# Optimization experiments

Hardware: AMD Instinct MI355X
Metric: run time of the kernel (lower is better)

The kernel has to match this reference:

```python
import jax, jax.numpy as jnp
import numpy as np

B, L = 2, 2048
D_MODEL, D_INNER, D_STATE, DT_RANK, D_CONV, DEPTH = 1024, 2048, 16, 64, 4, 2
EPS = 1e-5


def setup_inputs() -> dict:
    key = jax.random.key(0)
    ks = jax.random.split(key, 8)
    rn = lambda k, s, scale=0.02: jax.random.normal(k, s, jnp.float32) * scale
    return {
        "x": jax.random.normal(ks[0], (B, L, D_MODEL), jnp.float32),
        "x_size": L,  # truthiness flag only; unused in the math
        "norm_w": jnp.ones((DEPTH, D_MODEL), jnp.float32),
        "norm_b": jnp.zeros((DEPTH, D_MODEL), jnp.float32),
        "in_proj_w": rn(ks[1], (DEPTH, 2 * D_INNER, D_MODEL)),
        "conv_w": rn(ks[2], (DEPTH, D_INNER, 1, D_CONV), 0.1),
        "conv_b": jnp.zeros((DEPTH, D_INNER), jnp.float32),
        "x_proj_w": rn(ks[3], (DEPTH, DT_RANK + 2 * D_STATE, D_INNER)),
        "dt_proj_w": rn(ks[4], (DEPTH, D_INNER, DT_RANK), 0.1),
        "dt_proj_b": jnp.full((DEPTH, D_INNER), -4.0, jnp.float32),  # softplus -> small dt
        "A_log": jnp.broadcast_to(
            jnp.log(jnp.arange(1, D_STATE + 1, dtype=jnp.float32)), (DEPTH, D_INNER, D_STATE)
        ) + jnp.zeros((DEPTH, D_INNER, D_STATE), jnp.float32),
        "D": jnp.ones((DEPTH, D_INNER), jnp.float32),
        "out_proj_w": rn(ks[5], (DEPTH, D_MODEL, D_INNER)),
    }


def _layernorm(x, w, b):
    mu = x.mean(-1, keepdims=True)
    var = ((x - mu) ** 2).mean(-1, keepdims=True)
    return (x - mu) * jax.lax.rsqrt(var + EPS) * w + b


def _selective_scan(u, dt, A, Bm, Cm, Dp):
    # u, dt: (B, L, di); A: (di, n); Bm, Cm: (B, L, n); Dp: (di,)
    def step(h, inp):
        u_t, dt_t, B_t, C_t = inp  # (B,di), (B,di), (B,n), (B,n)
        dA = jnp.exp(dt_t[..., None] * A)                       # (B, di, n)
        h = dA * h + (dt_t * u_t)[..., None] * B_t[:, None, :]  # (B, di, n)
        y = jnp.einsum('bdn,bn->bd', h, C_t)
        return h, y

    h0 = jnp.zeros((u.shape[0], A.shape[0], A.shape[1]), u.dtype)
    xs = (u.swapaxes(0, 1), dt.swapaxes(0, 1), Bm.swapaxes(0, 1), Cm.swapaxes(0, 1))
    _, ys = jax.lax.scan(step, h0, xs)  # ys: (L, B, di)
    return ys.swapaxes(0, 1) + u * Dp


def _mamba(x, in_proj_w, conv_w, conv_b, x_proj_w, dt_proj_w, dt_proj_b, A_log, Dp, out_proj_w):
    xz = jnp.einsum('bld,ed->ble', x, in_proj_w)  # (B, L, 2*di)
    u, z = jnp.split(xz, 2, axis=-1)
    # causal depthwise conv1d, kernel D_CONV
    uc = jax.lax.conv_general_dilated(
        u.swapaxes(1, 2), conv_w, (1,), [(D_CONV - 1, 0)],
        feature_group_count=D_INNER, dimension_numbers=('NCH', 'OIH', 'NCH'))
    u = jax.nn.silu(uc.swapaxes(1, 2) + conv_b)
    x_dbl = jnp.einsum('bld,ed->ble', u, x_proj_w)
    dt_r, Bm, Cm = jnp.split(x_dbl, [DT_RANK, DT_RANK + D_STATE], axis=-1)
    dt = jax.nn.softplus(jnp.einsum('blr,dr->bld', dt_r, dt_proj_w) + dt_proj_b)
    A = -jnp.exp(A_log)
    y = _selective_scan(u, dt, A, Bm, Cm, Dp)
    y = y * jax.nn.silu(z)
    return jnp.einsum('bld,ed->ble', y, out_proj_w)


def reference(x, x_size, norm_w, norm_b, in_proj_w, conv_w, conv_b, x_proj_w,
              dt_proj_w, dt_proj_b, A_log, D, out_proj_w):
    # BasicLayer passes x_size as `residual` (non-None), so each Block reduces to
    # x <- Mamba(LN(x)); the returned residual is discarded by x = blk(...)[0].
    h = x
    for i in range(DEPTH):
        hn = _layernorm(h, norm_w[i], norm_b[i])
        h = _mamba(hn, in_proj_w[i], conv_w[i], conv_b[i], x_proj_w[i],
                   dt_proj_w[i], dt_proj_b[i], A_log[i], D[i], out_proj_w[i])
    return h
```

## Files before the change

kernel.cpp:

```cpp
#include <hip/hip_runtime.h>
#include <hip/hip_bf16.h>
#include <math.h>

#define BQ 2
#define LQ 2048
#define D_MODEL 1024
#define D_INNER 2048
#define D_STATE 16
#define DT_RANK 64
#define D_CONV 4
#define DEPTH 2
#define NCHUNK 64
#define CHUNK 32
#define XSPLITK 8
#define XKC (D_INNER / XSPLITK)
#define OSK 2

typedef __attribute__((ext_vector_type(8))) short short8v;
typedef __attribute__((ext_vector_type(4))) float f32x4;

__device__ __forceinline__ short f2bf(float f) {
    union { float f; unsigned u; } v; v.f = f;
    unsigned r = v.u + 0x7fffu + ((v.u >> 16) & 1u);
    return (short)(r >> 16);
}

__device__ __forceinline__ float bf2f(unsigned short s) {
    union { unsigned u; float f; } v; v.u = ((unsigned)s) << 16;
    return v.f;
}

__device__ __forceinline__ void async16(void* lds, const void* gp) {
    __builtin_amdgcn_global_load_lds(
        (const __attribute__((address_space(1))) void*)gp,
        (__attribute__((address_space(3))) void*)lds, 16, 0, 0);
}

__global__ __launch_bounds__(256) void layernorm_kernel(
    const float* __restrict__ x, const float* __restrict__ w,
    const float* __restrict__ b, short* __restrict__ out)
{
    __shared__ float red[8];
    int row = blockIdx.x;
    const float* xr = x + (size_t)row * D_MODEL;
    float v[4];
    float s = 0.f, sq = 0.f;
#pragma unroll
    for (int i = 0; i < 4; ++i) {
        v[i] = xr[threadIdx.x + i * 256];
        s += v[i];
        sq += v[i] * v[i];
    }
#pragma unroll
    for (int off = 32; off; off >>= 1) {
        s += __shfl_down(s, off, 64);
        sq += __shfl_down(sq, off, 64);
    }
    int wid = threadIdx.x >> 6, lane = threadIdx.x & 63;
    if (!lane) { red[wid] = s; red[4 + wid] = sq; }
    __syncthreads();
    s = red[0] + red[1] + red[2] + red[3];
    sq = red[4] + red[5] + red[6] + red[7];
    float mu = s * (1.f / D_MODEL);
    float var = sq * (1.f / D_MODEL) - mu * mu;
    float rstd = rsqrtf(var + 1e-5f);
#pragma unroll
    for (int i = 0; i < 4; ++i) {
        int c = threadIdx.x + i * 256;
        out[(size_t)row * D_MODEL + c] = f2bf((v[i] - mu) * rstd * w[c] + b[c]);
    }
}

__global__ __launch_bounds__(512) void gemm256_bf16_kernel(
    const short* __restrict__ A, const short* __restrict__ W,
    short* __restrict__ C, int M, int N, int K)
{
    __shared__ __align__(16) short lds[65536];
    const int tid = threadIdx.x;
    const int lane = tid & 63;
    const int w = tid >> 6;
    const int wr = w >> 2, wc = w & 3;

    int nbx = N >> 8;
    int nwg = (M >> 8) * nbx;
    int q = nwg >> 3;
    int wg = ((int)blockIdx.x & 7) * q + ((int)blockIdx.x >> 3);
    int bx = wg % nbx, by = wg / nbx;
    int bm = by << 8, bn = bx << 8;

    const int fr = lane & 15;
    const int kl = lane >> 4;
    const int srow = lane >> 3;
    const int schunk = (lane & 7) ^ (srow & 7);

    f32x4 acc[8][4] = {};
    short8v af[4][2], bfA[2][2], bfB[2][2];

    auto STAGE = [&](int isA, int buf, int half, int kt) {
        const short* gp = isA ? A : W;
        int tile0 = isA ? bm : bn;
        int base = (isA ? 0 : 32768) + (buf * 2 + half) * 8192;
        int ko = kt << 6;
#pragma unroll
        for (int s = 0; s < 2; ++s) {
            int row = half * 128 + s * 64 + w * 8 + srow;
            const short* src = gp + (size_t)(tile0 + row) * K + ko + schunk * 8;
            async16(&lds[base + s * 4096 + w * 512], src);
        }
    };

    auto LOAD_A = [&](int buf, int mh) {
        int abase = (buf * 2 + mh) * 8192;
#pragma unroll
        for (int i = 0; i < 4; ++i) {
            int rl = wr * 64 + i * 16 + fr;
            int rsw = rl & 7;
#pragma unroll
            for (int ks = 0; ks < 2; ++ks)
                af[i][ks] = *(const short8v*)&lds[abase + rl * 64 + (((ks * 4 + kl) ^ rsw) * 8)];
        }
    };
    auto LOAD_B = [&](int buf, int nh, short8v (&bf)[2][2]) {
        int bbase = 32768 + (buf * 2 + nh) * 8192;
#pragma unroll
        for (int j = 0; j < 2; ++j) {
            int rl = wc * 32 + j * 16 + fr;
            int rsw = rl & 7;
#pragma unroll
            for (int ks = 0; ks < 2; ++ks)
                bf[j][ks] = *(const short8v*)&lds[bbase + rl * 64 + (((ks * 4 + kl) ^ rsw) * 8)];
        }
    };
    auto MFMA_Q = [&](int mh, int nh, short8v (&bf)[2][2]) {
        __builtin_amdgcn_s_setprio(1);
#pragma unroll
        for (int i = 0; i < 4; ++i)
#pragma unroll
            for (int j = 0; j < 2; ++j)
#pragma unroll
                for (int ks = 0; ks < 2; ++ks)
                    acc[mh * 4 + i][nh * 2 + j] = __builtin_amdgcn_mfma_f32_16x16x32_bf16(
                        af[i][ks], bf[j][ks], acc[mh * 4 + i][nh * 2 + j], 0, 0, 0);
        __builtin_amdgcn_s_setprio(0);
    };

#define GBAR  __builtin_amdgcn_s_barrier(); __builtin_amdgcn_sched_barrier(0);
#define LGKM  asm volatile("s_waitcnt lgkmcnt(0)" ::: "memory"); __builtin_amdgcn_sched_barrier(0);

    STAGE(1, 0, 0, 0); STAGE(0, 0, 0, 0);
    STAGE(1, 0, 1, 0); STAGE(0, 0, 1, 0);
    STAGE(1, 1, 0, 1); STAGE(0, 1, 0, 1);

    int T = K >> 7;
    for (int t = 0; t < T; ++t) {
        int last = (t == T - 1);
        asm volatile("s_waitcnt vmcnt(4)" ::: "memory");
        STAGE(1, 1, 1, 2 * t + 1);
        GBAR;
        LOAD_A(0, 0); LOAD_B(0, 0, bfA);
        LGKM; MFMA_Q(0, 0, bfA);
        GBAR;
        STAGE(0, 1, 1, 2 * t + 1);
        GBAR;
        LOAD_B(0, 1, bfB);
        LGKM; MFMA_Q(0, 1, bfB);
        GBAR;
        if (!last) STAGE(1, 0, 0, 2 * t + 2);
        GBAR;
        LOAD_A(0, 1);
        LGKM; MFMA_Q(1, 1, bfB);
        GBAR;
        if (!last) STAGE(0, 0, 0, 2 * t + 2);
        GBAR;
        MFMA_Q(1, 0, bfA);
        GBAR;
        if (last) { asm volatile("s_waitcnt vmcnt(0)" ::: "memory"); }
        else      { asm volatile("s_waitcnt vmcnt(4)" ::: "memory"); }
        if (!last) STAGE(1, 0, 1, 2 * t + 2);
        GBAR;
        LOAD_A(1, 0); LOAD_B(1, 0, bfA);
        LGKM; MFMA_Q(0, 0, bfA);
        GBAR;
        if (!last) STAGE(0, 0, 1, 2 * t + 2);
        GBAR;
        LOAD_B(1, 1, bfB);
        LGKM; MFMA_Q(0, 1, bfB);
        GBAR;
        if (!last) STAGE(1, 1, 0, 2 * t + 3);
        GBAR;
        LOAD_A(1, 1);
        LGKM; MFMA_Q(1, 1, bfB);
        GBAR;
        if (!last) STAGE(0, 1, 0, 2 * t + 3);
        GBAR;
        MFMA_Q(1, 0, bfA);
        GBAR;
    }
#undef GBAR
#undef LGKM

    int cr = (lane >> 4) * 4, cc = lane & 15;
#pragma unroll
    for (int i8 = 0; i8 < 8; ++i8) {
        int mh = i8 >> 2, ii = i8 & 3;
        int row0 = bm + mh * 128 + wr * 64 + ii * 16 + cr;
#pragma unroll
        for (int p = 0; p < 4; ++p) {
            short* Cp = C + (size_t)(row0 + p) * N + bn;
#pragma unroll
            for (int j4 = 0; j4 < 4; ++j4) {
                int nh = j4 >> 1, jj = j4 & 1;
                Cp[nh * 128 + wc * 32 + jj * 16 + cc] = f2bf(acc[i8][j4][p]);
            }
        }
    }
}

__global__ __launch_bounds__(256) void gemm_bf16_kernel(
    const short* __restrict__ A, const short* __restrict__ W,
    void* __restrict__ Cv, int M, int N, int K,
    const float* __restrict__ bias, int epilogue, int nsk)
{
    __shared__ __align__(16) short As[2][128 * 64];
    __shared__ __align__(16) short Bs[2][128 * 64];
    int tid = threadIdx.x;
    int lane = tid & 63, wv = tid >> 6;
    int nbx = N >> 7;
    int nwg = (M >> 7) * nbx;
    int ntot = nwg * nsk;
    int q = ntot >> 3;
    int wgz = ((int)blockIdx.x & 7) * q + ((int)blockIdx.x >> 3);
    int sk = wgz / nwg;
    int wg = wgz % nwg;
    int bx = wg % nbx, by = wg / nbx;
    int bm = by * 128, bn = bx * 128;
    int wr = wv >> 1, wc = wv & 1;
    int Kl = K / nsk;
    int koff = sk * Kl;

    const int fr = lane & 15;
    const int kl = lane >> 4;
    const int srow = lane >> 3;
    const int schunk = (lane & 7) ^ (srow & 7);

    f32x4 acc[4][4] = {};

    const short* Ab = A + (size_t)bm * K + koff;
    const short* Bb = W + (size_t)bn * K + koff;

    auto STAGE = [&](int buf, int kt) {
        int ko = kt << 6;
#pragma unroll
        for (int s = 0; s < 4; ++s) {
            int row = s * 32 + wv * 8 + srow;
            async16(&As[buf][s * 2048 + wv * 512], Ab + (size_t)row * K + ko + schunk * 8);
            async16(&Bs[buf][s * 2048 + wv * 512], Bb + (size_t)row * K + ko + schunk * 8);
        }
    };

    int NT = Kl >> 6;
    STAGE(0, 0);
    if (NT > 1) STAGE(1, 1);

    for (int t = 0; t < NT; ++t) {
        if (t + 1 < NT) { asm volatile("s_waitcnt vmcnt(8)" ::: "memory"); }
        else            { asm volatile("s_waitcnt vmcnt(0)" ::: "memory"); }
        __builtin_amdgcn_s_barrier();
        __builtin_amdgcn_sched_barrier(0);
        int buf = t & 1;
        short8v af[4][2], bf[4][2];
#pragma unroll
        for (int i = 0; i < 4; ++i) {
            int rl = wr * 64 + i * 16 + fr;
            int rsw = rl & 7;
#pragma unroll
            for (int ks = 0; ks < 2; ++ks)
                af[i][ks] = *(const short8v*)&As[buf][rl * 64 + (((ks * 4 + kl) ^ rsw) * 8)];
        }
#pragma unroll
        for (int j = 0; j < 4; ++j) {
            int rl = wc * 64 + j * 16 + fr;
            int rsw = rl & 7;
#pragma unroll
            for (int ks = 0; ks < 2; ++ks)
                bf[j][ks] = *(const short8v*)&Bs[buf][rl * 64 + (((ks * 4 + kl) ^ rsw) * 8)];
        }
        asm volatile("s_waitcnt lgkmcnt(0)" ::: "memory");
        __builtin_amdgcn_sched_barrier(0);
        __builtin_amdgcn_s_setprio(1);
#pragma unroll
        for (int i = 0; i < 4; ++i)
#pragma unroll
            for (int j = 0; j < 4; ++j)
#pragma unroll
                for (int ks = 0; ks < 2; ++ks)
                    acc[i][j] = __builtin_amdgcn_mfma_f32_16x16x32_bf16(
                        af[i][ks], bf[j][ks], acc[i][j], 0, 0, 0);
        __builtin_amdgcn_s_setprio(0);
        __builtin_amdgcn_s_barrier();
        __builtin_amdgcn_sched_barrier(0);
        if (t + 2 < NT) STAGE(buf, t + 2);
    }

    int cr = (lane >> 4) * 4, cc = lane & 15;
    size_t skoff = (size_t)sk * M * N;
#pragma unroll
    for (int i = 0; i < 4; ++i)
#pragma unroll
        for (int p = 0; p < 4; ++p) {
            int row = bm + wr * 64 + i * 16 + cr + p;
#pragma unroll
            for (int j = 0; j < 4; ++j) {
                int col = bn + wc * 64 + cc + j * 16;
                float v = acc[i][j][p];
                if (epilogue == 2)
                    ((short*)Cv)[(size_t)row * N + col] = f2bf(v);
                else
                    ((float*)Cv)[skoff + (size_t)row * N + col] = v;
            }
        }
}

__global__ __launch_bounds__(256) void osum_kernel(
    const float* __restrict__ P, float* __restrict__ out)
{
    size_t i = ((size_t)blockIdx.x * 256 + threadIdx.x) * 4;
    float4 a = *(const float4*)(P + i);
    float4 b = *(const float4*)(P + (size_t)BQ * LQ * D_MODEL + i);
    a.x += b.x; a.y += b.y; a.z += b.z; a.w += b.w;
    *(float4*)(out + i) = a;
}

__global__ __launch_bounds__(256) void dtproj_kernel(
    const short* __restrict__ A, const short* __restrict__ W,
    const float* __restrict__ bias, short* __restrict__ Out)
{
    int lane = threadIdx.x & 63, w = threadIdx.x >> 6;
    int m0 = blockIdx.y * 64 + w * 16;
    int bn = blockIdx.x * 128;
    int fr = lane & 15, fk = (lane >> 4) * 8;
    const short* Ap = A + (size_t)(m0 + fr) * DT_RANK + fk;
    short8v a0 = *(const short8v*)(Ap);
    short8v a1 = *(const short8v*)(Ap + 32);
    f32x4 acc[8] = {};
#pragma unroll
    for (int j = 0; j < 8; ++j) {
        const short* Wp = W + (size_t)(bn + j * 16 + fr) * DT_RANK + fk;
        short8v b0 = *(const short8v*)(Wp);
        short8v b1 = *(const short8v*)(Wp + 32);
        acc[j] = __builtin_amdgcn_mfma_f32_16x16x32_bf16(a0, b0, acc[j], 0, 0, 0);
        acc[j] = __builtin_amdgcn_mfma_f32_16x16x32_bf16(a1, b1, acc[j], 0, 0, 0);
    }
    int cr = (lane >> 4) * 4, cc = lane & 15;
#pragma unroll
    for (int j = 0; j < 8; ++j) {
        int col = bn + j * 16 + cc;
        float bv = bias[col];
#pragma unroll
        for (int p = 0; p < 4; ++p) {
            float v = acc[j][p] + bv;
            v = (v > 20.f) ? v : __logf(1.f + __expf(v));
            Out[(size_t)(m0 + cr + p) * D_INNER + col] = f2bf(v);
        }
    }
}

__global__ __launch_bounds__(256) void xproj_kernel(
    const short* __restrict__ A, const short* __restrict__ W,
    float* __restrict__ Xpart)
{
    int lane = threadIdx.x & 63, wv = threadIdx.x >> 6;
    int sk = blockIdx.x;
    int m0 = blockIdx.y * 64 + wv * 16;
    int fr = lane & 15, fk = (lane >> 4) * 8;
    const short* Ap = A + (size_t)(m0 + fr) * D_INNER + sk * XKC + fk;
    const short* Wp = W + (size_t)fr * D_INNER + sk * XKC + fk;
    f32x4 acc[6] = {};
    for (int k = 0; k < XKC; k += 32) {
        short8v af = *(const short8v*)(Ap + k);
#pragma unroll
        for (int j = 0; j < 6; ++j) {
            short8v bf = *(const short8v*)(Wp + (size_t)j * 16 * D_INNER + k);
            acc[j] = __builtin_amdgcn_mfma_f32_16x16x32_bf16(af, bf, acc[j], 0, 0, 0);
        }
    }
    int cr = (lane >> 4) * 4, cc = lane & 15;
    float* Op = Xpart + ((size_t)sk * (BQ * LQ) + m0 + cr) * 96 + cc;
#pragma unroll
    for (int j = 0; j < 6; ++j)
#pragma unroll
        for (int p = 0; p < 4; ++p)
            Op[(size_t)p * 96 + j * 16] = acc[j][p];
}

__global__ __launch_bounds__(256) void xreduce_kernel(
    const float* __restrict__ Xpart, float* __restrict__ xdbl,
    short* __restrict__ dtr)
{
    size_t i = (size_t)blockIdx.x * 256 + threadIdx.x;
    float s = 0.f;
#pragma unroll
    for (int sk = 0; sk < XSPLITK; ++sk)
        s += Xpart[(size_t)sk * ((size_t)BQ * LQ * 96) + i];
    xdbl[i] = s;
    int col = (int)(i % 96);
    if (col < DT_RANK)
        dtr[(i / 96) * DT_RANK + col] = f2bf(s);
}

__global__ __launch_bounds__(256) void conv_silu_kernel(
    const unsigned short* __restrict__ uz, short* __restrict__ outb,
    const float* __restrict__ w, const float* __restrict__ bias)
{
    int idx = blockIdx.x * 256 + threadIdx.x;
    int c = idx & (D_INNER - 1);
    int bl = idx / D_INNER;
    int l = bl & (LQ - 1);
    int b = bl / LQ;
    float acc = bias[c];
#pragma unroll
    for (int k = 0; k < D_CONV; ++k) {
        int ls = l - (D_CONV - 1) + k;
        if (ls >= 0)
            acc += bf2f(uz[((size_t)b * LQ + ls) * (2 * D_INNER) + c]) * w[c * D_CONV + k];
    }
    float val = acc / (1.f + __expf(-acc));
    outb[idx] = f2bf(val);
}

__global__ __launch_bounds__(256) void scan_phase1_kernel(
    const unsigned short* __restrict__ u, const unsigned short* __restrict__ dt,
    const float* __restrict__ xdbl, const float* __restrict__ A_log,
    float* __restrict__ Pbuf, float* __restrict__ Fbuf)
{
    __shared__ float S[CHUNK][D_STATE];
    int t = threadIdx.x;
    int d = blockIdx.x * 256 + t;
    int c = blockIdx.y;
    int b = blockIdx.z;
    int l0 = c * CHUNK;
    {
        int row = t >> 3, cc2 = (t & 7) * 2;
        const float* src = xdbl + ((size_t)(b * LQ + l0 + row)) * 96 + DT_RANK + cc2;
        *(float2*)&S[row][cc2] = *(const float2*)src;
    }
    float A[D_STATE], h[D_STATE];
    {
        const float4* ap = (const float4*)(A_log + (size_t)d * D_STATE);
#pragma unroll
        for (int g = 0; g < 4; ++g) {
            float4 a = ap[g];
            A[g*4+0] = -__expf(a.x); A[g*4+1] = -__expf(a.y);
            A[g*4+2] = -__expf(a.z); A[g*4+3] = -__expf(a.w);
        }
    }
#pragma unroll
    for (int n = 0; n < D_STATE; ++n) h[n] = 0.f;
    float dtsum = 0.f;
    const unsigned short* up  = u  + ((size_t)b * LQ + l0) * D_INNER + d;
    const unsigned short* dtp = dt + ((size_t)b * LQ + l0) * D_INNER + d;
    __syncthreads();

    for (int lb = 0; lb < CHUNK; lb += 8) {
        float uvv[8], dtvv[8];
#pragma unroll
        for (int i = 0; i < 8; ++i) {
            uvv[i]  = bf2f(up [(size_t)(lb + i) * D_INNER]);
            dtvv[i] = bf2f(dtp[(size_t)(lb + i) * D_INNER]);
        }
#pragma unroll
        for (int i = 0; i < 8; ++i) {
            int l = lb + i;
            float dtv = dtvv[i];
            float du = dtv * uvv[i];
            dtsum += dtv;
#pragma unroll
            for (int n4 = 0; n4 < D_STATE; n4 += 4) {
                float4 Bv = *(const float4*)&S[l][n4];
                float bb[4] = {Bv.x, Bv.y, Bv.z, Bv.w};
#pragma unroll
                for (int k = 0; k < 4; ++k) {
                    int n = n4 + k;
                    float dA = __expf(dtv * A[n]);
                    h[n] = dA * h[n] + du * bb[k];
                }
            }
        }
    }
    size_t base = ((size_t)(b * NCHUNK + c) * D_STATE) * D_INNER + d;
#pragma unroll
    for (int n = 0; n < D_STATE; ++n) {
        Pbuf[base + (size_t)n * D_INNER] = __expf(A[n] * dtsum);
        Fbuf[base + (size_t)n * D_INNER] = h[n];
    }
}

__global__ __launch_bounds__(256) void scan_phase2_kernel(
    const float* __restrict__ Pbuf, float* __restrict__ Fbuf)
{
    int d = blockIdx.x * 256 + threadIdx.x;
    int n = blockIdx.y;
    int b = blockIdx.z;
    float hinit = 0.f;
    for (int c = 0; c < NCHUNK; ++c) {
        size_t idx = ((size_t)(b * NCHUNK + c) * D_STATE + n) * D_INNER + d;
        float P = Pbuf[idx];
        float F = Fbuf[idx];
        Fbuf[idx] = hinit;
        hinit = P * hinit + F;
    }
}

__global__ __launch_bounds__(256) void scan_phase3_kernel(
    const unsigned short* __restrict__ u, const unsigned short* __restrict__ dt,
    const float* __restrict__ xdbl, const float* __restrict__ A_log,
    const float* __restrict__ Dp, const float* __restrict__ Hinit,
    const unsigned short* __restrict__ uz, short* __restrict__ yout)
{
    __shared__ float S[CHUNK][32];
    int t = threadIdx.x;
    int d = blockIdx.x * 256 + t;
    int c = blockIdx.y;
    int b = blockIdx.z;
    int l0 = c * CHUNK;
    {
        int row = t >> 3, cg = (t & 7) * 4;
        const float* src = xdbl + ((size_t)(b * LQ + l0 + row)) * 96 + DT_RANK + cg;
        *(float4*)&S[row][cg ^ ((row & 7) << 2)] = *(const float4*)src;
    }
    float A[D_STATE], h[D_STATE];
    {
        const float4* ap = (const float4*)(A_log + (size_t)d * D_STATE);
#pragma unroll
        for (int g = 0; g < 4; ++g) {
            float4 a = ap[g];
            A[g*4+0] = -__expf(a.x); A[g*4+1] = -__expf(a.y);
            A[g*4+2] = -__expf(a.z); A[g*4+3] = -__expf(a.w);
        }
    }
    size_t base = ((size_t)(b * NCHUNK + c) * D_STATE) * D_INNER + d;
#pragma unroll
    for (int n = 0; n < D_STATE; ++n)
        h[n] = Hinit[base + (size_t)n * D_INNER];
    float Dd = Dp[d];
    const unsigned short* up  = u  + ((size_t)b * LQ + l0) * D_INNER + d;
    const unsigned short* dtp = dt + ((size_t)b * LQ + l0) * D_INNER + d;
    const unsigned short* zp = uz + ((size_t)b * LQ + l0) * (2 * D_INNER) + D_INNER + d;
    short* yp = yout + ((size_t)b * LQ + l0) * D_INNER + d;
    __syncthreads();

    for (int lb = 0; lb < CHUNK; lb += 8) {
        float uvv[8], dtvv[8], zvv[8];
#pragma unroll
        for (int i = 0; i < 8; ++i) {
            uvv[i]  = bf2f(up [(size_t)(lb + i) * D_INNER]);
            dtvv[i] = bf2f(dtp[(size_t)(lb + i) * D_INNER]);
            zvv[i]  = bf2f(zp [(size_t)(lb + i) * (2 * D_INNER)]);
        }
#pragma unroll
        for (int i = 0; i < 8; ++i) {
            int l = lb + i;
            float dtv = dtvv[i];
            float du = dtv * uvv[i];
            float acc = 0.f;
            int sw = (l & 7) << 2;
#pragma unroll
            for (int n4 = 0; n4 < D_STATE; n4 += 4) {
                float4 Bv = *(const float4*)&S[l][n4 ^ sw];
                float4 Cv = *(const float4*)&S[l][(16 + n4) ^ sw];
                float bb[4] = {Bv.x, Bv.y, Bv.z, Bv.w};
                float cc[4] = {Cv.x, Cv.y, Cv.z, Cv.w};
#pragma unroll
                for (int k = 0; k < 4; ++k) {
                    int n = n4 + k;
                    float dA = __expf(dtv * A[n]);
                    h[n] = dA * h[n] + du * bb[k];
                    acc += h[n] * cc[k];
                }
            }
            float y = acc + uvv[i] * Dd;
            float zv = zvv[i];
            float g = zv / (1.f + __expf(-zv));
            yp[(size_t)l * D_INNER] = f2bf(y * g);
        }
    }
}

__global__ __launch_bounds__(256) void convert_all_kernel(
    const float* __restrict__ w_in, const float* __restrict__ w_out,
    const float* __restrict__ w_xp, const float* __restrict__ w_dt,
    short* __restrict__ wbuf)
{
    const int IN_B  = (2 * D_INNER * D_MODEL) / 1024;
    const int OUT_B = (D_MODEL * D_INNER) / 1024;
    const int XP_B  = (96 * D_INNER) / 1024;
    int blk = blockIdx.x;
    const float* src; short* dst;
    if (blk < IN_B)                 { src = w_in;  dst = wbuf; }
    else if (blk < IN_B + OUT_B)    { src = w_out; dst = wbuf + 2 * D_INNER * D_MODEL; blk -= IN_B; }
    else if (blk < IN_B + OUT_B + XP_B) { src = w_xp; dst = wbuf + 2 * D_INNER * D_MODEL + D_MODEL * D_INNER; blk -= IN_B + OUT_B; }
    else { src = w_dt; dst = wbuf + 2 * D_INNER * D_MODEL + D_MODEL * D_INNER + 96 * D_INNER; blk -= IN_B + OUT_B + XP_B; }
    int i = blk * 1024 + threadIdx.x * 4;
    float4 v = *(const float4*)(src + i);
    short4 o = make_short4(f2bf(v.x), f2bf(v.y), f2bf(v.z), f2bf(v.w));
    *(short4*)(dst + i) = o;
}

extern "C" void kernel_launch(void* const* d_in, const int* in_sizes, int n_in,
                              void* d_out, int out_size, void* d_ws, size_t ws_size,
                              hipStream_t stream)
{
    const float* x        = (const float*)d_in[0];
    const float* norm_w   = (const float*)d_in[2];
    const float* norm_b   = (const float*)d_in[3];
    const float* in_proj  = (const float*)d_in[4];
    const float* conv_w   = (const float*)d_in[5];
    const float* conv_b   = (const float*)d_in[6];
    const float* x_proj   = (const float*)d_in[7];
    const float* dt_proj  = (const float*)d_in[8];
    const float* dt_projb = (const float*)d_in[9];
    const float* A_log    = (const float*)d_in[10];
    const float* Dp       = (const float*)d_in[11];
    const float* out_proj = (const float*)d_in[12];
    float* out = (float*)d_out;
    float* ws  = (float*)d_ws;

    const size_t BL   = (size_t)BQ * LQ;
    const size_t BLDM = BL * D_MODEL;
    const size_t BLDI = BL * D_INNER;
    const int IN_W  = 2 * D_INNER * D_MODEL;
    const int OUT_W = D_MODEL * D_INNER;
    const int XP_W  = 96 * D_INNER;
    const int DT_W  = D_INNER * DT_RANK;
    const int CV_BLOCKS = (IN_W + OUT_W + XP_W + DT_W) / 1024;

    size_t o = 0;
    float* Pbuf  = ws + o; o += BLDM;
    short* uzb   = (short*)(ws + o); o += BL * 2 * D_INNER / 2;
    short* dtb   = (short*)(ws + o); o += BLDI / 2;
    float* xdbl  = ws + o; o += BL * 96;
    float* h1    = ws + o; o += BLDM;
    float* Fbuf  = ws + o; o += BLDM;
    short* ucx   = (short*)(ws + o); o += BLDI / 2;
    short* dtr   = (short*)(ws + o); o += BL * DT_RANK / 2;
    float* Opart = ws + o; o += (size_t)OSK * BLDM;
    short* wbuf  = (short*)(ws + o);
    o += (size_t)(IN_W + OUT_W + XP_W + DT_W + 1) / 2;

    short* hnb = (short*)Pbuf;
    float* Xpart = h1;

    for (int layer = 0; layer < DEPTH; ++layer) {
        const float* src = (layer == 0) ? x : h1;
        float* dst = (layer == DEPTH - 1) ? out : h1;

        layernorm_kernel<<<(int)BL, 256, 0, stream>>>(
            src, norm_w + (size_t)layer * D_MODEL, norm_b + (size_t)layer * D_MODEL, hnb);

        convert_all_kernel<<<CV_BLOCKS, 256, 0, stream>>>(
            in_proj + (size_t)layer * IN_W, out_proj + (size_t)layer * OUT_W,
            x_proj + (size_t)layer * XP_W, dt_proj + (size_t)layer * DT_W, wbuf);

        gemm256_bf16_kernel<<<(int)(BL / 256) * (2 * D_INNER / 256), 512, 0, stream>>>(
            hnb, wbuf, uzb, (int)BL, 2 * D_INNER, D_MODEL);

        conv_silu_kernel<<<(int)(BLDI / 256), 256, 0, stream>>>(
            (const unsigned short*)uzb, ucx,
            conv_w + (size_t)layer * D_INNER * D_CONV,
            conv_b + (size_t)layer * D_INNER);

        xproj_kernel<<<dim3(XSPLITK, BL / 64), 256, 0, stream>>>(
            ucx, wbuf + IN_W + OUT_W, Xpart);
        xreduce_kernel<<<(int)(BL * 96 / 256), 256, 0, stream>>>(Xpart, xdbl, dtr);

        dtproj_kernel<<<dim3(D_INNER / 128, BL / 64), 256, 0, stream>>>(
            dtr, wbuf + IN_W + OUT_W + XP_W,
            dt_projb + (size_t)layer * D_INNER, dtb);

        const float* Al = A_log + (size_t)layer * D_INNER * D_STATE;
        scan_phase1_kernel<<<dim3(D_INNER / 256, NCHUNK, BQ), 256, 0, stream>>>(
            (const unsigned short*)ucx, (const unsigned short*)dtb, xdbl, Al, Pbuf, Fbuf);
        scan_phase2_kernel<<<dim3(D_INNER / 256, D_STATE, BQ), 256, 0, stream>>>(
            Pbuf, Fbuf);
        scan_phase3_kernel<<<dim3(D_INNER / 256, NCHUNK, BQ), 256, 0, stream>>>(
            (const unsigned short*)ucx, (const unsigned short*)dtb, xdbl, Al,
            Dp + (size_t)layer * D_INNER, Fbuf,
            (const unsigned short*)uzb, (short*)ucx);

        gemm_bf16_kernel<<<(int)(BL / 128) * (D_MODEL / 128) * OSK, 256, 0, stream>>>(
            ucx, wbuf + IN_W, Opart, (int)BL, D_MODEL, D_INNER, nullptr, 0, OSK);
        osum_kernel<<<(int)(BLDM / 1024), 256, 0, stream>>>(Opart, dst);
    }
}
```

Before: 484.0 us.

## Fuse split-K output sum with next-layer layernorm; drop Pbuf, vectorize conv

For the inter-layer boundary, the split-K partial sum of the out-projection is fused with the next layer's layernorm, so the fp32 hidden state is never written and reread. The scan no longer stores a per-state decay buffer. Phase 1 writes one dtsum per channel and chunk, and phase 2 recomputes exp(A*dtsum), which trades memory traffic for extra exp work. The conv+SiLU kernel now handles two channels per thread with 32-bit loads and stores, and the workspace layout is reorganized to match.

```diff
diff --git a/kernel.cpp b/kernel.cpp
--- a/kernel.cpp
+++ b/kernel.cpp
@@ -48,6 +48,43 @@
 #pragma unroll
     for (int i = 0; i < 4; ++i) {
         v[i] = xr[threadIdx.x + i * 256];
+        s += v[i];
+        sq += v[i] * v[i];
+    }
+#pragma unroll
+    for (int off = 32; off; off >>= 1) {
+        s += __shfl_down(s, off, 64);
+        sq += __shfl_down(sq, off, 64);
+    }
+    int wid = threadIdx.x >> 6, lane = threadIdx.x & 63;
+    if (!lane) { red[wid] = s; red[4 + wid] = sq; }
+    __syncthreads();
+    s = red[0] + red[1] + red[2] + red[3];
+    sq = red[4] + red[5] + red[6] + red[7];
+    float mu = s * (1.f / D_MODEL);
+    float var = sq * (1.f / D_MODEL) - mu * mu;
+    float rstd = rsqrtf(var + 1e-5f);
+#pragma unroll
+    for (int i = 0; i < 4; ++i) {
+        int c = threadIdx.x + i * 256;
+        out[(size_t)row * D_MODEL + c] = f2bf((v[i] - mu) * rstd * w[c] + b[c]);
+    }
+}
+
+__global__ __launch_bounds__(256) void osum_ln_kernel(
+    const float* __restrict__ P, const float* __restrict__ w,
+    const float* __restrict__ b, short* __restrict__ out)
+{
+    __shared__ float red[8];
+    int row = blockIdx.x;
+    const float* p0 = P + (size_t)row * D_MODEL;
+    const float* p1 = P + (size_t)BQ * LQ * D_MODEL + (size_t)row * D_MODEL;
+    float v[4];
+    float s = 0.f, sq = 0.f;
+#pragma unroll
+    for (int i = 0; i < 4; ++i) {
+        int c = threadIdx.x + i * 256;
+        v[i] = p0[c] + p1[c];
         s += v[i];
         sq += v[i] * v[i];
     }
@@ -413,25 +450,38 @@
     const float* __restrict__ w, const float* __restrict__ bias)
 {
     int idx = blockIdx.x * 256 + threadIdx.x;
-    int c = idx & (D_INNER - 1);
-    int bl = idx / D_INNER;
+    int e0 = idx * 2;
+    int c = e0 & (D_INNER - 1);
+    int bl = e0 / D_INNER;
     int l = bl & (LQ - 1);
     int b = bl / LQ;
-    float acc = bias[c];
+    float acc0 = bias[c], acc1 = bias[c + 1];
+    float w0[D_CONV], w1[D_CONV];
+#pragma unroll
+    for (int k = 0; k < D_CONV; ++k) {
+        w0[k] = w[c * D_CONV + k];
+        w1[k] = w[(c + 1) * D_CONV + k];
+    }
 #pragma unroll
     for (int k = 0; k < D_CONV; ++k) {
         int ls = l - (D_CONV - 1) + k;
-        if (ls >= 0)
-            acc += bf2f(uz[((size_t)b * LQ + ls) * (2 * D_INNER) + c]) * w[c * D_CONV + k];
-    }
-    float val = acc / (1.f + __expf(-acc));
-    outb[idx] = f2bf(val);
+        if (ls >= 0) {
+            unsigned v = *(const unsigned*)&uz[((size_t)b * LQ + ls) * (2 * D_INNER) + c];
+            acc0 += bf2f((unsigned short)(v & 0xffff)) * w0[k];
+            acc1 += bf2f((unsigned short)(v >> 16)) * w1[k];
+        }
+    }
+    float v0 = acc0 / (1.f + __expf(-acc0));
+    float v1 = acc1 / (1.f + __expf(-acc1));
+    unsigned o = (unsigned)(unsigned short)f2bf(v0) |
+                 ((unsigned)(unsigned short)f2bf(v1) << 16);
+    *(unsigned*)&outb[e0] = o;
 }
 
 __global__ __launch_bounds__(256) void scan_phase1_kernel(
     const unsigned short* __restrict__ u, const unsigned short* __restrict__ dt,
     const float* __restrict__ xdbl, const float* __restrict__ A_log,
-    float* __restrict__ Pbuf, float* __restrict__ Fbuf)
+    float* __restrict__ dtsumb, float* __restrict__ Fbuf)
 {
     __shared__ float S[CHUNK][D_STATE];
     int t = threadIdx.x;
@@ -487,25 +537,26 @@
             }
         }
     }
+    dtsumb[(size_t)(b * NCHUNK + c) * D_INNER + d] = dtsum;
     size_t base = ((size_t)(b * NCHUNK + c) * D_STATE) * D_INNER + d;
 #pragma unroll
-    for (int n = 0; n < D_STATE; ++n) {
-        Pbuf[base + (size_t)n * D_INNER] = __expf(A[n] * dtsum);
+    for (int n = 0; n < D_STATE; ++n)
         Fbuf[base + (size_t)n * D_INNER] = h[n];
-    }
 }
 
 __global__ __launch_bounds__(256) void scan_phase2_kernel(
-    const float* __restrict__ Pbuf, float* __restrict__ Fbuf)
+    const float* __restrict__ dtsumb, const float* __restrict__ A_log,
+    float* __restrict__ Fbuf)
 {
     int d = blockIdx.x * 256 + threadIdx.x;
     int n = blockIdx.y;
     int b = blockIdx.z;
+    float A = -__expf(A_log[(size_t)d * D_STATE + n]);
     float hinit = 0.f;
     for (int c = 0; c < NCHUNK; ++c) {
         size_t idx = ((size_t)(b * NCHUNK + c) * D_STATE + n) * D_INNER + d;
-        float P = Pbuf[idx];
         float F = Fbuf[idx];
+        float P = __expf(A * dtsumb[(size_t)(b * NCHUNK + c) * D_INNER + d]);
         Fbuf[idx] = hinit;
         hinit = P * hinit + F;
     }
@@ -635,27 +686,23 @@
     const int CV_BLOCKS = (IN_W + OUT_W + XP_W + DT_W) / 1024;
 
     size_t o = 0;
-    float* Pbuf  = ws + o; o += BLDM;
+    short* hnb   = (short*)(ws + o); o += BLDM / 2;
     short* uzb   = (short*)(ws + o); o += BL * 2 * D_INNER / 2;
     short* dtb   = (short*)(ws + o); o += BLDI / 2;
     float* xdbl  = ws + o; o += BL * 96;
-    float* h1    = ws + o; o += BLDM;
+    float* Xpart = ws + o; o += (size_t)XSPLITK * BL * 96;
     float* Fbuf  = ws + o; o += BLDM;
+    float* dtsumb = ws + o; o += (size_t)BQ * NCHUNK * D_INNER;
     short* ucx   = (short*)(ws + o); o += BLDI / 2;
     short* dtr   = (short*)(ws + o); o += BL * DT_RANK / 2;
     float* Opart = ws + o; o += (size_t)OSK * BLDM;
     short* wbuf  = (short*)(ws + o);
     o += (size_t)(IN_W + OUT_W + XP_W + DT_W + 1) / 2;
 
-    short* hnb = (short*)Pbuf;
-    float* Xpart = h1;
-
     for (int layer = 0; layer < DEPTH; ++layer) {
-        const float* src = (layer == 0) ? x : h1;
-        float* dst = (layer == DEPTH - 1) ? out : h1;
-
-        layernorm_kernel<<<(int)BL, 256, 0, stream>>>(
-            src, norm_w + (size_t)layer * D_MODEL, norm_b + (size_t)layer * D_MODEL, hnb);
+        if (layer == 0)
+            layernorm_kernel<<<(int)BL, 256, 0, stream>>>(
+                x, norm_w, norm_b, hnb);
 
         convert_all_kernel<<<CV_BLOCKS, 256, 0, stream>>>(
             in_proj + (size_t)layer * IN_W, out_proj + (size_t)layer * OUT_W,
@@ -664,7 +711,7 @@
         gemm256_bf16_kernel<<<(int)(BL / 256) * (2 * D_INNER / 256), 512, 0, stream>>>(
             hnb, wbuf, uzb, (int)BL, 2 * D_INNER, D_MODEL);
 
-        conv_silu_kernel<<<(int)(BLDI / 256), 256, 0, stream>>>(
+        conv_silu_kernel<<<(int)(BLDI / 512), 256, 0, stream>>>(
             (const unsigned short*)uzb, ucx,
             conv_w + (size_t)layer * D_INNER * D_CONV,
             conv_b + (size_t)layer * D_INNER);
@@ -679,9 +726,10 @@
 
         const float* Al = A_log + (size_t)layer * D_INNER * D_STATE;
         scan_phase1_kernel<<<dim3(D_INNER / 256, NCHUNK, BQ), 256, 0, stream>>>(
-            (const unsigned short*)ucx, (const unsigned short*)dtb, xdbl, Al, Pbuf, Fbuf);
+            (const unsigned short*)ucx, (const unsigned short*)dtb, xdbl, Al,
+            dtsumb, Fbuf);
         scan_phase2_kernel<<<dim3(D_INNER / 256, D_STATE, BQ), 256, 0, stream>>>(
-            Pbuf, Fbuf);
+            dtsumb, Al, Fbuf);
         scan_phase3_kernel<<<dim3(D_INNER / 256, NCHUNK, BQ), 256, 0, stream>>>(
             (const unsigned short*)ucx, (const unsigned short*)dtb, xdbl, Al,
             Dp + (size_t)layer * D_INNER, Fbuf,
@@ -689,6 +737,12 @@
 
         gemm_bf16_kernel<<<(int)(BL / 128) * (D_MODEL / 128) * OSK, 256, 0, stream>>>(
             ucx, wbuf + IN_W, Opart, (int)BL, D_MODEL, D_INNER, nullptr, 0, OSK);
-        osum_kernel<<<(int)(BLDM / 1024), 256, 0, stream>>>(Opart, dst);
-    }
-}
+
+        if (layer == DEPTH - 1)
+            osum_kernel<<<(int)(BLDM / 1024), 256, 0, stream>>>(Opart, out);
+        else
+            osum_ln_kernel<<<(int)BL, 256, 0, stream>>>(
+                Opart, norm_w + (size_t)(layer + 1) * D_MODEL,
+                norm_b + (size_t)(layer + 1) * D_MODEL, hnb);
+    }
+}
```

Result: faster. 447.7 us (-7.5%).
